# Optimization experiments

Measured on AMD Instinct MI355X. Metric: run time of the kernel, lower is better.

The kernel has to match this reference:

```python
import jax, jax.numpy as jnp
import numpy as np

N = 2048          # batch*trg_len (B=4, T=512)
B, T = 4, 512
D = 512           # model_dim
V = 32000         # vocab_size
K = 16            # top_k


def setup_inputs() -> dict:
    key = jax.random.key(0)
    ks = jax.random.split(key, 12)
    hidden = jax.random.normal(ks[0], (N, D), dtype=jnp.float32)
    logits = jax.random.normal(ks[1], (N, V), dtype=jnp.float32)
    distances = jax.random.uniform(ks[2], (N, K), dtype=jnp.float32)  # L2 distances >= 0
    searched_hidden = jax.random.normal(ks[3], (N, K, D), dtype=jnp.float32)
    token_indices = jax.random.randint(ks[4], (N, K), 0, V, dtype=jnp.int64)
    s = 1.0 / np.sqrt(2 * D)
    # bandwidth estimator: Linear(2D -> 1), bias init 20 for GaussianKernel
    bw_W = jax.random.uniform(ks[5], (2 * D, 1), minval=-s, maxval=s, dtype=jnp.float32)
    bw_b = jnp.array([20.0], dtype=jnp.float32)
    # mixing weight estimator: Linear(2D->D), ReLU, Linear(D->1)
    mw_W1 = jax.random.uniform(ks[6], (2 * D, D), minval=-s, maxval=s, dtype=jnp.float32)
    mw_b1 = jax.random.uniform(ks[7], (D,), minval=-s, maxval=s, dtype=jnp.float32)
    s2 = 1.0 / np.sqrt(D)
    mw_W2 = jax.random.uniform(ks[8], (D, 1), minval=-s2, maxval=s2, dtype=jnp.float32)
    mw_b2 = jax.random.uniform(ks[9], (1,), minval=-s2, maxval=s2, dtype=jnp.float32)
    return {
        "hidden": hidden, "logits": logits, "distances": distances,
        "searched_hidden": searched_hidden, "token_indices": token_indices,
        "bw_W": bw_W, "bw_b": bw_b,
        "mw_W1": mw_W1, "mw_b1": mw_b1, "mw_W2": mw_W2, "mw_b2": mw_b2,
    }


def reference(hidden, logits, distances, searched_hidden, token_indices,
              bw_W, bw_b, mw_W1, mw_b1, mw_W2, mw_b2):
    # --- bandwidth: sigmoid(Linear([hidden, mean_k searched_hidden])) -> [N, 1]
    mean_hidden = searched_hidden.mean(axis=1)                       # [N, D]
    bw_in = jnp.concatenate([hidden, mean_hidden], axis=-1)          # [N, 2D]
    bandwidth = jax.nn.sigmoid(bw_in @ bw_W + bw_b)                  # [N, 1]

    # --- model distribution over vocab
    model_dist = jax.nn.softmax(logits, axis=-1)                     # [N, V]

    # --- Gaussian kernel, index_type 'L2': scores = -distances / bandwidth
    scores = -distances / bandwidth                                  # [N, K]
    sparse_dist = jax.nn.softmax(scores, axis=-1)                    # [N, K]
    # scatter-add sparse probs into vocab-sized distribution
    rows = jnp.arange(N)[:, None]                                    # [N, 1]
    example_dist = jnp.zeros((N, V), dtype=sparse_dist.dtype).at[rows, token_indices].add(sparse_dist)

    # --- mixing weight MLP on [hidden, prob-weighted searched hidden]
    merged = jnp.einsum('nkd,nk->nd', searched_hidden, sparse_dist)  # [N, D]
    mw_in = jnp.concatenate([hidden, merged], axis=-1)               # [N, 2D]
    h1 = jax.nn.relu(mw_in @ mw_W1 + mw_b1)                          # [N, D]
    mixing = jax.nn.sigmoid(h1 @ mw_W2 + mw_b2)                      # [N, 1]

    mixed = (1.0 - mixing) * model_dist + mixing * example_dist      # [N, V]
    log_probs = jnp.log(mixed).reshape(B, T, V)
    return log_probs
```

## Files before the change

kernel.cpp:

```cpp
#include <hip/hip_runtime.h>
#include <math.h>

#define N_ROWS 2048
#define D_DIM  512
#define V_DIM  32000
#define K_TOP  16

__global__ __launch_bounds__(512) void k_mlp(
    const float* __restrict__ hidden,
    const float* __restrict__ sh,
    const float* __restrict__ dist,
    const float* __restrict__ bwW,
    const float* __restrict__ bwb,
    const float* __restrict__ W1,
    const float* __restrict__ b1,
    const float* __restrict__ W2,
    const float* __restrict__ b2,
    float* __restrict__ sd_out,
    float* __restrict__ mix_out,
    float* __restrict__ l1m_out)
{
  __shared__ float smem[8192];
  __shared__ float4 psum[4][128];
  __shared__ float sd_l[8][K_TOP];
  __shared__ float redb[2];
  const int tid = threadIdx.x;
  const int q   = tid & 127;
  const int kg  = tid >> 7;
  const int tx  = tid & 63;
  const int tz  = tid >> 6;
  const int r0  = blockIdx.x * 8;

  const float4* bwW4 = (const float4*)bwW;

  for (int r = 0; r < 8; ++r) {
    const int row = r0 + r;
    const float4* sh4 = (const float4*)(sh + (size_t)row * (K_TOP * D_DIM));
    float4 shv[4];
    float4 s4 = make_float4(0.f, 0.f, 0.f, 0.f);
#pragma unroll
    for (int kk = 0; kk < 4; ++kk) {
      shv[kk] = sh4[(kk * 4 + kg) * 128 + q];
      s4.x += shv[kk].x; s4.y += shv[kk].y; s4.z += shv[kk].z; s4.w += shv[kk].w;
    }
    psum[kg][q] = s4;
    __syncthreads();
    if (kg == 0) {
      float4 m4;
      m4.x = psum[0][q].x + psum[1][q].x + psum[2][q].x + psum[3][q].x;
      m4.y = psum[0][q].y + psum[1][q].y + psum[2][q].y + psum[3][q].y;
      m4.z = psum[0][q].z + psum[1][q].z + psum[2][q].z + psum[3][q].z;
      m4.w = psum[0][q].w + psum[1][q].w + psum[2][q].w + psum[3][q].w;
      const float4 h4 = ((const float4*)(hidden + (size_t)row * D_DIM))[q];
      ((float4*)smem)[r * 256 + q] = h4;
      const float4 w0 = bwW4[q];
      const float4 w1 = bwW4[128 + q];
      float bp = h4.x * w0.x + h4.y * w0.y + h4.z * w0.z + h4.w * w0.w
               + 0.0625f * (m4.x * w1.x + m4.y * w1.y + m4.z * w1.z + m4.w * w1.w);
#pragma unroll
      for (int off = 32; off > 0; off >>= 1) bp += __shfl_down(bp, off);
      if ((tid & 63) == 0) redb[tid >> 6] = bp;
    }
    __syncthreads();
    if (tid == 0) {
      const float dot = redb[0] + redb[1] + bwb[0];
      const float bw  = 1.0f / (1.0f + __expf(-dot));
      float sc[K_TOP];
      float mx = -1e30f;
#pragma unroll
      for (int k = 0; k < K_TOP; ++k) {
        sc[k] = -dist[row * K_TOP + k] / bw;
        mx = fmaxf(mx, sc[k]);
      }
      float ssum = 0.0f;
#pragma unroll
      for (int k = 0; k < K_TOP; ++k) { sc[k] = __expf(sc[k] - mx); ssum += sc[k]; }
      const float inv = 1.0f / ssum;
#pragma unroll
      for (int k = 0; k < K_TOP; ++k) {
        const float v = sc[k] * inv;
        sd_l[r][k] = v;
        sd_out[row * K_TOP + k] = v;
      }
    }
    __syncthreads();
    float4 mg = make_float4(0.f, 0.f, 0.f, 0.f);
#pragma unroll
    for (int kk = 0; kk < 4; ++kk) {
      const float s = sd_l[r][kk * 4 + kg];
      mg.x = fmaf(s, shv[kk].x, mg.x); mg.y = fmaf(s, shv[kk].y, mg.y);
      mg.z = fmaf(s, shv[kk].z, mg.z); mg.w = fmaf(s, shv[kk].w, mg.w);
    }
    psum[kg][q] = mg;
    __syncthreads();
    if (kg == 0) {
      float4 m4;
      m4.x = psum[0][q].x + psum[1][q].x + psum[2][q].x + psum[3][q].x;
      m4.y = psum[0][q].y + psum[1][q].y + psum[2][q].y + psum[3][q].y;
      m4.z = psum[0][q].z + psum[1][q].z + psum[2][q].z + psum[3][q].z;
      m4.w = psum[0][q].w + psum[1][q].w + psum[2][q].w + psum[3][q].w;
      ((float4*)smem)[r * 256 + 128 + q] = m4;
    }
    __syncthreads();
  }

  float acc[8][8];
#pragma unroll
  for (int r = 0; r < 8; ++r)
#pragma unroll
    for (int j = 0; j < 8; ++j) acc[r][j] = 0.0f;

  const float4* A4 = (const float4*)smem;
  const float4* W4 = (const float4*)W1;
  const int kbase = tz * 128;
  for (int kk = 0; kk < 128; kk += 4) {
    const int k0 = kbase + kk;
    float4 a[8];
#pragma unroll
    for (int r = 0; r < 8; ++r) a[r] = A4[r * 256 + (k0 >> 2)];
#pragma unroll
    for (int dk = 0; dk < 4; ++dk) {
      const int k = k0 + dk;
      const float4 wlo = W4[k * 128 + tx * 2];
      const float4 whi = W4[k * 128 + tx * 2 + 1];
#pragma unroll
      for (int r = 0; r < 8; ++r) {
        const float av = (dk == 0) ? a[r].x : (dk == 1) ? a[r].y
                       : (dk == 2) ? a[r].z : a[r].w;
        acc[r][0] = fmaf(av, wlo.x, acc[r][0]);
        acc[r][1] = fmaf(av, wlo.y, acc[r][1]);
        acc[r][2] = fmaf(av, wlo.z, acc[r][2]);
        acc[r][3] = fmaf(av, wlo.w, acc[r][3]);
        acc[r][4] = fmaf(av, whi.x, acc[r][4]);
        acc[r][5] = fmaf(av, whi.y, acc[r][5]);
        acc[r][6] = fmaf(av, whi.z, acc[r][6]);
        acc[r][7] = fmaf(av, whi.w, acc[r][7]);
      }
    }
  }
  __syncthreads();

#define RED_WRITE(set) {                                                     \
  _Pragma("unroll") for (int r = 0; r < 8; ++r) {                            \
    _Pragma("unroll") for (int j = 0; j < 8; ++j) {                          \
      smem[(set) * 4096 + r * 512 + tx + (j << 6)] = acc[r][j]; } } }
#define RED_ADD(set) {                                                       \
  _Pragma("unroll") for (int r = 0; r < 8; ++r) {                            \
    _Pragma("unroll") for (int j = 0; j < 8; ++j) {                          \
      acc[r][j] += smem[(set) * 4096 + r * 512 + tx + (j << 6)]; } } }

  if (tz == 4) { RED_WRITE(0) } else if (tz == 5) { RED_WRITE(1) }
  __syncthreads();
  if (tz == 0) { RED_ADD(0) } else if (tz == 1) { RED_ADD(1) }
  __syncthreads();
  if (tz == 6) { RED_WRITE(0) } else if (tz == 7) { RED_WRITE(1) }
  __syncthreads();
  if (tz == 2) { RED_ADD(0) } else if (tz == 3) { RED_ADD(1) }
  __syncthreads();
  if (tz == 2) { RED_WRITE(0) } else if (tz == 3) { RED_WRITE(1) }
  __syncthreads();
  if (tz == 0) { RED_ADD(0) } else if (tz == 1) { RED_ADD(1) }
  __syncthreads();
  if (tz == 1) { RED_WRITE(0) }
  __syncthreads();

  if (tz == 0) {
    RED_ADD(0)
    const float4* b1v = (const float4*)b1;
    const float4* w2v = (const float4*)W2;
    const float4 blo = b1v[tx * 2], bhi = b1v[tx * 2 + 1];
    const float4 wlo = w2v[tx * 2], whi = w2v[tx * 2 + 1];
#pragma unroll
    for (int r = 0; r < 8; ++r) {
      float s = fmaxf(acc[r][0] + blo.x, 0.f) * wlo.x
              + fmaxf(acc[r][1] + blo.y, 0.f) * wlo.y
              + fmaxf(acc[r][2] + blo.z, 0.f) * wlo.z
              + fmaxf(acc[r][3] + blo.w, 0.f) * wlo.w
              + fmaxf(acc[r][4] + bhi.x, 0.f) * whi.x
              + fmaxf(acc[r][5] + bhi.y, 0.f) * whi.y
              + fmaxf(acc[r][6] + bhi.z, 0.f) * whi.z
              + fmaxf(acc[r][7] + bhi.w, 0.f) * whi.w;
#pragma unroll
      for (int off = 32; off > 0; off >>= 1) s += __shfl_down(s, off);
      if (tx == 0) {
        const float x  = s + b2[0];
        const float mg = 1.0f / (1.0f + __expf(-x));
        mix_out[r0 + r] = mg;
        l1m_out[r0 + r] = logf(1.0f - mg);
      }
    }
  }
#undef RED_WRITE
#undef RED_ADD
}

__global__ __launch_bounds__(1024) void k_out(
    const float* __restrict__ logits,
    const float* __restrict__ sd,
    const float* __restrict__ mix,
    const float* __restrict__ l1m,
    const int* __restrict__ tok,
    float* __restrict__ out)
{
  const int n   = blockIdx.x;
  const int tid = threadIdx.x;
  __shared__ float Ms[16], Ss[16];
  __shared__ float cSh, LSh;

  const float4* in4 = (const float4*)(logits + (size_t)n * V_DIM);
  float4*      out4 = (float4*)(out + (size_t)n * V_DIM);

  float4 v[8];
  float tmax = -1e30f;
#pragma unroll
  for (int i = 0; i < 8; ++i) {
    const int idx = tid + (i << 10);
    if (idx < 8000) v[i] = in4[idx];
    else            v[i] = make_float4(-1e30f, -1e30f, -1e30f, -1e30f);
    tmax = fmaxf(tmax, fmaxf(fmaxf(v[i].x, v[i].y), fmaxf(v[i].z, v[i].w)));
  }
  float tsum = 0.0f;
#pragma unroll
  for (int i = 0; i < 8; ++i) {
    tsum += __expf(v[i].x - tmax) + __expf(v[i].y - tmax)
          + __expf(v[i].z - tmax) + __expf(v[i].w - tmax);
  }
#pragma unroll
  for (int off = 32; off > 0; off >>= 1) {
    const float M2 = __shfl_xor(tmax, off);
    const float S2 = __shfl_xor(tsum, off);
    const float Mn = fmaxf(tmax, M2);
    tsum = tsum * __expf(tmax - Mn) + S2 * __expf(M2 - Mn);
    tmax = Mn;
  }
  if ((tid & 63) == 0) { Ms[tid >> 6] = tmax; Ss[tid >> 6] = tsum; }
  __syncthreads();
  if (tid == 0) {
    float M = Ms[0], S = Ss[0];
#pragma unroll
    for (int w = 1; w < 16; ++w) {
      const float Mn = fmaxf(M, Ms[w]);
      S = S * __expf(M - Mn) + Ss[w] * __expf(Ms[w] - Mn);
      M = Mn;
    }
    const float L = M + logf(S);
    LSh = L;
    cSh = l1m[n] - L;
  }
  __syncthreads();
  const float c = cSh;
#pragma unroll
  for (int i = 0; i < 8; ++i) {
    const int idx = tid + (i << 10);
    if (idx < 8000) {
      float4 o;
      o.x = v[i].x + c; o.y = v[i].y + c; o.z = v[i].z + c; o.w = v[i].w + c;
      out4[idx] = o;
    }
  }
  __syncthreads();
  if (tid < K_TOP) {
    const int k  = tid;
    const int my = tok[n * K_TOP + k];
    float e = 0.0f;
    bool first = true;
#pragma unroll
    for (int k2 = 0; k2 < K_TOP; ++k2) {
      const int i2 = tok[n * K_TOP + k2];
      if (i2 == my) { e += sd[n * K_TOP + k2]; if (k2 < k) first = false; }
    }
    if (first) {
      const float x = logits[(size_t)n * V_DIM + my];
      const float m = mix[n];
      const float p = __expf(x - LSh);
      out[(size_t)n * V_DIM + my] = logf((1.0f - m) * p + m * e);
    }
  }
}

extern "C" void kernel_launch(void* const* d_in, const int* in_sizes, int n_in,
                              void* d_out, int out_size, void* d_ws, size_t ws_size,
                              hipStream_t stream)
{
  const float* hidden = (const float*)d_in[0];
  const float* logits = (const float*)d_in[1];
  const float* dist   = (const float*)d_in[2];
  const float* sh     = (const float*)d_in[3];
  const int*   tok    = (const int*)d_in[4];
  const float* bwW    = (const float*)d_in[5];
  const float* bwb    = (const float*)d_in[6];
  const float* W1     = (const float*)d_in[7];
  const float* b1     = (const float*)d_in[8];
  const float* W2     = (const float*)d_in[9];
  const float* b2     = (const float*)d_in[10];
  float* out = (float*)d_out;
  float* ws  = (float*)d_ws;

  float* sdp = ws;
  float* mxp = ws + N_ROWS * K_TOP;
  float* l1p = mxp + N_ROWS;

  k_mlp<<<N_ROWS / 8, 512, 0, stream>>>(hidden, sh, dist, bwW, bwb,
                                        W1, b1, W2, b2, sdp, mxp, l1p);
  k_out<<<N_ROWS, 1024, 0, stream>>>(logits, sdp, mxp, l1p, tok, out);
}
```

Measured before the change: 167.4 us.

## Give each wavefront its own row in MLP prologue and use nontemporal loads and stores

The k_mlp prologue no longer walks the 8 rows one after another with several block-wide barriers per row. Each of the 8 wavefronts now handles one row by itself, with warp-shuffle reductions and a redundant per-lane softmax, so only one barrier is left. k_out prefetches the token-index fixup inputs before the main pass and uses nontemporal loads and stores for the streaming logits and output, to reduce cache pollution. The prologue re-reads searched_hidden twice per lane, and all 64 lanes do the same softmax work.

```diff
diff --git a/kernel.cpp b/kernel.cpp
--- a/kernel.cpp
+++ b/kernel.cpp
@@ -5,6 +5,8 @@
 #define D_DIM  512
 #define V_DIM  32000
 #define K_TOP  16
+
+typedef float f32x4 __attribute__((ext_vector_type(4)));
 
 __global__ __launch_bounds__(512) void k_mlp(
     const float* __restrict__ hidden,
@@ -21,88 +23,73 @@
     float* __restrict__ l1m_out)
 {
   __shared__ float smem[8192];
-  __shared__ float4 psum[4][128];
-  __shared__ float sd_l[8][K_TOP];
-  __shared__ float redb[2];
   const int tid = threadIdx.x;
-  const int q   = tid & 127;
-  const int kg  = tid >> 7;
   const int tx  = tid & 63;
   const int tz  = tid >> 6;
   const int r0  = blockIdx.x * 8;
 
-  const float4* bwW4 = (const float4*)bwW;
-
-  for (int r = 0; r < 8; ++r) {
-    const int row = r0 + r;
-    const float4* sh4 = (const float4*)(sh + (size_t)row * (K_TOP * D_DIM));
-    float4 shv[4];
-    float4 s4 = make_float4(0.f, 0.f, 0.f, 0.f);
-#pragma unroll
-    for (int kk = 0; kk < 4; ++kk) {
-      shv[kk] = sh4[(kk * 4 + kg) * 128 + q];
-      s4.x += shv[kk].x; s4.y += shv[kk].y; s4.z += shv[kk].z; s4.w += shv[kk].w;
-    }
-    psum[kg][q] = s4;
-    __syncthreads();
-    if (kg == 0) {
-      float4 m4;
-      m4.x = psum[0][q].x + psum[1][q].x + psum[2][q].x + psum[3][q].x;
-      m4.y = psum[0][q].y + psum[1][q].y + psum[2][q].y + psum[3][q].y;
-      m4.z = psum[0][q].z + psum[1][q].z + psum[2][q].z + psum[3][q].z;
-      m4.w = psum[0][q].w + psum[1][q].w + psum[2][q].w + psum[3][q].w;
-      const float4 h4 = ((const float4*)(hidden + (size_t)row * D_DIM))[q];
-      ((float4*)smem)[r * 256 + q] = h4;
-      const float4 w0 = bwW4[q];
-      const float4 w1 = bwW4[128 + q];
-      float bp = h4.x * w0.x + h4.y * w0.y + h4.z * w0.z + h4.w * w0.w
-               + 0.0625f * (m4.x * w1.x + m4.y * w1.y + m4.z * w1.z + m4.w * w1.w);
-#pragma unroll
-      for (int off = 32; off > 0; off >>= 1) bp += __shfl_down(bp, off);
-      if ((tid & 63) == 0) redb[tid >> 6] = bp;
-    }
-    __syncthreads();
-    if (tid == 0) {
-      const float dot = redb[0] + redb[1] + bwb[0];
-      const float bw  = 1.0f / (1.0f + __expf(-dot));
-      float sc[K_TOP];
-      float mx = -1e30f;
-#pragma unroll
-      for (int k = 0; k < K_TOP; ++k) {
-        sc[k] = -dist[row * K_TOP + k] / bw;
-        mx = fmaxf(mx, sc[k]);
-      }
-      float ssum = 0.0f;
-#pragma unroll
-      for (int k = 0; k < K_TOP; ++k) { sc[k] = __expf(sc[k] - mx); ssum += sc[k]; }
-      const float inv = 1.0f / ssum;
-#pragma unroll
-      for (int k = 0; k < K_TOP; ++k) {
-        const float v = sc[k] * inv;
-        sd_l[r][k] = v;
-        sd_out[row * K_TOP + k] = v;
-      }
-    }
-    __syncthreads();
-    float4 mg = make_float4(0.f, 0.f, 0.f, 0.f);
-#pragma unroll
-    for (int kk = 0; kk < 4; ++kk) {
-      const float s = sd_l[r][kk * 4 + kg];
-      mg.x = fmaf(s, shv[kk].x, mg.x); mg.y = fmaf(s, shv[kk].y, mg.y);
-      mg.z = fmaf(s, shv[kk].z, mg.z); mg.w = fmaf(s, shv[kk].w, mg.w);
-    }
-    psum[kg][q] = mg;
-    __syncthreads();
-    if (kg == 0) {
-      float4 m4;
-      m4.x = psum[0][q].x + psum[1][q].x + psum[2][q].x + psum[3][q].x;
-      m4.y = psum[0][q].y + psum[1][q].y + psum[2][q].y + psum[3][q].y;
-      m4.z = psum[0][q].z + psum[1][q].z + psum[2][q].z + psum[3][q].z;
-      m4.w = psum[0][q].w + psum[1][q].w + psum[2][q].w + psum[3][q].w;
-      ((float4*)smem)[r * 256 + 128 + q] = m4;
-    }
-    __syncthreads();
-  }
+  {
+    const int lane = tx;
+    const int row  = r0 + tz;
+    const float4* sh4  = (const float4*)(sh + (size_t)row * (K_TOP * D_DIM));
+    const float4* hid4 = (const float4*)(hidden + (size_t)row * D_DIM);
+    const float4* bwW4 = (const float4*)bwW;
+
+    float4 msA = make_float4(0.f,0.f,0.f,0.f), msB = make_float4(0.f,0.f,0.f,0.f);
+#pragma unroll
+    for (int k = 0; k < K_TOP; ++k) {
+      const float4 a = sh4[k * 128 + lane];
+      const float4 b = sh4[k * 128 + 64 + lane];
+      msA.x += a.x; msA.y += a.y; msA.z += a.z; msA.w += a.w;
+      msB.x += b.x; msB.y += b.y; msB.z += b.z; msB.w += b.w;
+    }
+    const float4 h4a = hid4[lane], h4b = hid4[64 + lane];
+    float4* A4w = (float4*)smem;
+    A4w[tz * 256 + lane]      = h4a;
+    A4w[tz * 256 + 64 + lane] = h4b;
+    const float4 wa = bwW4[lane],       wb = bwW4[64 + lane];
+    const float4 wc = bwW4[128 + lane], wd = bwW4[192 + lane];
+    float bp = h4a.x*wa.x + h4a.y*wa.y + h4a.z*wa.z + h4a.w*wa.w
+             + h4b.x*wb.x + h4b.y*wb.y + h4b.z*wb.z + h4b.w*wb.w
+             + 0.0625f * (msA.x*wc.x + msA.y*wc.y + msA.z*wc.z + msA.w*wc.w
+                        + msB.x*wd.x + msB.y*wd.y + msB.z*wd.z + msB.w*wd.w);
+#pragma unroll
+    for (int off = 32; off > 0; off >>= 1) bp += __shfl_down(bp, off);
+    bp = __shfl(bp, 0);
+    const float bw = 1.0f / (1.0f + __expf(-(bp + bwb[0])));
+
+    float sc[K_TOP];
+    float mx = -1e30f;
+#pragma unroll
+    for (int k = 0; k < K_TOP; ++k) {
+      sc[k] = -dist[row * K_TOP + k] / bw;
+      mx = fmaxf(mx, sc[k]);
+    }
+    float ssum = 0.0f;
+#pragma unroll
+    for (int k = 0; k < K_TOP; ++k) { sc[k] = __expf(sc[k] - mx); ssum += sc[k]; }
+    const float inv = 1.0f / ssum;
+#pragma unroll
+    for (int k = 0; k < K_TOP; ++k) sc[k] *= inv;
+    if (lane == 0) {
+#pragma unroll
+      for (int k = 0; k < K_TOP; ++k) sd_out[row * K_TOP + k] = sc[k];
+    }
+
+    float4 mgA = make_float4(0.f,0.f,0.f,0.f), mgB = make_float4(0.f,0.f,0.f,0.f);
+#pragma unroll
+    for (int k = 0; k < K_TOP; ++k) {
+      const float4 a = sh4[k * 128 + lane];
+      const float4 b = sh4[k * 128 + 64 + lane];
+      mgA.x = fmaf(sc[k], a.x, mgA.x); mgA.y = fmaf(sc[k], a.y, mgA.y);
+      mgA.z = fmaf(sc[k], a.z, mgA.z); mgA.w = fmaf(sc[k], a.w, mgA.w);
+      mgB.x = fmaf(sc[k], b.x, mgB.x); mgB.y = fmaf(sc[k], b.y, mgB.y);
+      mgB.z = fmaf(sc[k], b.z, mgB.z); mgB.w = fmaf(sc[k], b.w, mgB.w);
+    }
+    A4w[tz * 256 + 128 + lane] = mgA;
+    A4w[tz * 256 + 192 + lane] = mgB;
+  }
+  __syncthreads();
 
   float acc[8][8];
 #pragma unroll
@@ -207,16 +194,30 @@
   __shared__ float Ms[16], Ss[16];
   __shared__ float cSh, LSh;
 
-  const float4* in4 = (const float4*)(logits + (size_t)n * V_DIM);
-  float4*      out4 = (float4*)(out + (size_t)n * V_DIM);
-
-  float4 v[8];
+  float fx_x = 0.f, fx_e = 0.f, fx_m = 0.f;
+  int fx_my = 0; bool fx_first = false;
+  if (tid < K_TOP) {
+    fx_my = tok[n * K_TOP + tid];
+    fx_first = true;
+#pragma unroll
+    for (int k2 = 0; k2 < K_TOP; ++k2) {
+      const int i2 = tok[n * K_TOP + k2];
+      if (i2 == fx_my) { fx_e += sd[n * K_TOP + k2]; if (k2 < tid) fx_first = false; }
+    }
+    fx_x = logits[(size_t)n * V_DIM + fx_my];
+    fx_m = mix[n];
+  }
+
+  const f32x4* in4 = (const f32x4*)(logits + (size_t)n * V_DIM);
+  f32x4*      out4 = (f32x4*)(out + (size_t)n * V_DIM);
+
+  f32x4 v[8];
   float tmax = -1e30f;
 #pragma unroll
   for (int i = 0; i < 8; ++i) {
     const int idx = tid + (i << 10);
-    if (idx < 8000) v[i] = in4[idx];
-    else            v[i] = make_float4(-1e30f, -1e30f, -1e30f, -1e30f);
+    if (idx < 8000) v[i] = __builtin_nontemporal_load(in4 + idx);
+    else { v[i].x = -1e30f; v[i].y = -1e30f; v[i].z = -1e30f; v[i].w = -1e30f; }
     tmax = fmaxf(tmax, fmaxf(fmaxf(v[i].x, v[i].y), fmaxf(v[i].z, v[i].w)));
   }
   float tsum = 0.0f;
@@ -253,28 +254,16 @@
   for (int i = 0; i < 8; ++i) {
     const int idx = tid + (i << 10);
     if (idx < 8000) {
-      float4 o;
+      f32x4 o;
       o.x = v[i].x + c; o.y = v[i].y + c; o.z = v[i].z + c; o.w = v[i].w + c;
-      out4[idx] = o;
-    }
-  }
-  __syncthreads();
-  if (tid < K_TOP) {
-    const int k  = tid;
-    const int my = tok[n * K_TOP + k];
-    float e = 0.0f;
-    bool first = true;
-#pragma unroll
-    for (int k2 = 0; k2 < K_TOP; ++k2) {
-      const int i2 = tok[n * K_TOP + k2];
-      if (i2 == my) { e += sd[n * K_TOP + k2]; if (k2 < k) first = false; }
-    }
-    if (first) {
-      const float x = logits[(size_t)n * V_DIM + my];
-      const float m = mix[n];
-      const float p = __expf(x - LSh);
-      out[(size_t)n * V_DIM + my] = logf((1.0f - m) * p + m * e);
-    }
+      __builtin_nontemporal_store(o, out4 + idx);
+    }
+  }
+  __syncthreads();
+  if (tid < K_TOP && fx_first) {
+    const float p = __expf(fx_x - LSh);
+    const float r = logf((1.0f - fx_m) * p + fx_m * fx_e);
+    __builtin_nontemporal_store(r, out + (size_t)n * V_DIM + fx_my);
   }
 }
 
```

New measurement: 149.8 us. 10.5% less time.
